# Kernel optimization log

Measured on AMD Instinct MI355X. Metric: run time of the kernel, lower is better.

Reference implementation:

```python
import jax, jax.numpy as jnp
import numpy as np

K = 3        # kernel size
PAD = 1      # padding
DG = 16      # deformable groups
MAXR = 10.0  # max_residue_magnitude


def _lrelu(x):
    return jnp.where(x >= 0, x, 0.1 * x)


def _conv3(x, w, b):
    y = jax.lax.conv_general_dilated(x, w, (1, 1), 'SAME',
                                     dimension_numbers=('NCHW', 'OIHW', 'NCHW'))
    return y + b[None, :, None, None]


def _deform_conv2d(x, offset, mask, weight, bias):
    # x: [B,Cin,H,W]; offset: [B,2*DG*K*K,H,W]; mask: [B,DG*K*K,H,W]
    B, Cin, H, W = x.shape
    Cout = weight.shape[0]
    G, Cg, K2 = DG, Cin // DG, K * K
    off = offset.reshape(B, G, K2, 2, H, W)
    dy, dx = off[:, :, :, 0], off[:, :, :, 1]
    ky = jnp.repeat(jnp.arange(K), K).astype(x.dtype)   # [K2]
    kx = jnp.tile(jnp.arange(K), K).astype(x.dtype)
    hh = jnp.arange(H, dtype=x.dtype)
    ww = jnp.arange(W, dtype=x.dtype)
    # sampling positions [B,G,K2,H,W]
    py = dy + ky[None, None, :, None, None] + hh[None, None, None, :, None] - PAD
    px = dx + kx[None, None, :, None, None] + ww[None, None, None, None, :] - PAD
    y0 = jnp.floor(py)
    x0 = jnp.floor(px)
    wy1 = py - y0
    wx1 = px - x0
    xf = x.reshape(B, G, Cg, H * W)

    def gather(yi, xi, wgt):
        valid = (yi >= 0) & (yi <= H - 1) & (xi >= 0) & (xi <= W - 1)
        idx = (jnp.clip(yi, 0, H - 1).astype(jnp.int32) * W
               + jnp.clip(xi, 0, W - 1).astype(jnp.int32)).reshape(B, G, -1)
        vals = jnp.take_along_axis(
            xf, jnp.broadcast_to(idx[:, :, None, :], (B, G, Cg, idx.shape[-1])), axis=3)
        vals = vals.reshape(B, G, Cg, K2, H, W)
        w = (wgt * valid.astype(x.dtype))[:, :, None]  # [B,G,1,K2,H,W]
        return vals * w

    s = (gather(y0, x0, (1 - wy1) * (1 - wx1))
         + gather(y0, x0 + 1, (1 - wy1) * wx1)
         + gather(y0 + 1, x0, wy1 * (1 - wx1))
         + gather(y0 + 1, x0 + 1, wy1 * wx1))
    s = s * mask.reshape(B, G, K2, H, W)[:, :, None]
    wr = weight.reshape(Cout, G, Cg, K2)
    out = jnp.einsum('ogck,bgckhw->bohw', wr, s)
    return out + bias[None, :, None, None]


def setup_inputs() -> dict:
    key = jax.random.key(0)
    ks = jax.random.split(key, 16)
    B, Cin, Cout, H, W = 4, 128, 64, 96, 96
    Coff = 3 * Cout + 4  # 196
    stdv = 1.0 / np.sqrt(Cin * K * K)
    inp = {
        'x': jax.random.normal(ks[0], (B, Cin, H, W), jnp.float32),
        'extra_feat': jax.random.normal(ks[1], (B, 3 * Cout, H, W), jnp.float32),
        'flow_1': jax.random.normal(ks[2], (B, 2, H, W), jnp.float32),
        'flow_2': jax.random.normal(ks[3], (B, 2, H, W), jnp.float32),
        'weight': jax.random.uniform(ks[4], (Cout, Cin, K, K), jnp.float32, -stdv, stdv),
        'bias': jax.random.normal(ks[5], (Cout,), jnp.float32) * 0.01,
        'ow0': jax.random.normal(ks[6], (Cout, Coff, K, K), jnp.float32) * 0.02,
        'ob0': jnp.zeros((Cout,), jnp.float32),
        'ow1': jax.random.normal(ks[7], (Cout, Cout, K, K), jnp.float32) * 0.02,
        'ob1': jnp.zeros((Cout,), jnp.float32),
        'ow2': jax.random.normal(ks[8], (Cout, Cout, K, K), jnp.float32) * 0.02,
        'ob2': jnp.zeros((Cout,), jnp.float32),
        'ow3': jax.random.normal(ks[9], (27 * DG, Cout, K, K), jnp.float32) * 0.01,
        'ob3': jnp.zeros((27 * DG,), jnp.float32),
    }
    return inp


def reference(x, extra_feat, flow_1, flow_2, weight, bias,
              ow0, ob0, ow1, ob1, ow2, ob2, ow3, ob3):
    feat = jnp.concatenate([extra_feat, flow_1, flow_2], axis=1)
    h = _lrelu(_conv3(feat, ow0, ob0))
    h = _lrelu(_conv3(h, ow1, ob1))
    h = _lrelu(_conv3(h, ow2, ob2))
    out = _conv3(h, ow3, ob3)
    o1, o2, m = jnp.split(out, 3, axis=1)
    offs = MAXR * jnp.tanh(jnp.concatenate([o1, o2], axis=1))
    off1, off2 = jnp.split(offs, 2, axis=1)
    off1 = off1 + jnp.tile(flow_1[:, ::-1], (1, off1.shape[1] // 2, 1, 1))
    off2 = off2 + jnp.tile(flow_2[:, ::-1], (1, off2.shape[1] // 2, 1, 1))
    offset = jnp.concatenate([off1, off2], axis=1)
    mask = jax.nn.sigmoid(m)
    return _deform_conv2d(x, offset, mask, weight, bias)
```

## Files before the change

kernel.cpp:

```cpp
#include <hip/hip_runtime.h>
#include <math.h>

#define HW 9216
#define Hh 96
#define Ww 96
#define PHW 9604

typedef __attribute__((ext_vector_type(8))) short bh8;
typedef __attribute__((ext_vector_type(4))) short bh4;
typedef __attribute__((ext_vector_type(4))) float f32x4;
typedef __attribute__((ext_vector_type(2))) float f32x2;
typedef __attribute__((ext_vector_type(4))) int i32x4;
union bh8i { bh8 v; i32x4 i; };

__device__ __forceinline__ short f2bf(float f) {
    union { float f; unsigned u; } v; v.f = f;
    unsigned r = v.u + 0x7FFFu + ((v.u >> 16) & 1u);
    return (short)(r >> 16);
}
__device__ __forceinline__ float bf2f(short s) {
    union { unsigned u; float f; } v; v.u = ((unsigned)(unsigned short)s) << 16;
    return v.f;
}
__device__ __forceinline__ float lo_bf(unsigned u) {
    union { unsigned u; float f; } v; v.u = u << 16; return v.f;
}
__device__ __forceinline__ float hi_bf(unsigned u) {
    union { unsigned u; float f; } v; v.u = u & 0xFFFF0000u; return v.f;
}
__device__ __forceinline__ int cvt_pk_bf16(float lo, float hi) {
    int r;
    asm("v_cvt_pk_bf16_f32 %0, %1, %2" : "=v"(r) : "v"(lo), "v"(hi));
    return r;
}

__global__ void prep_misc(short* __restrict__ xpad1, short* __restrict__ hpa,
                          short* __restrict__ hpb, short* __restrict__ xdp,
                          const float* __restrict__ ow0, const float* __restrict__ ow1,
                          const float* __restrict__ ow2, const float* __restrict__ ow3,
                          const float* __restrict__ wd,
                          short* __restrict__ wb0, short* __restrict__ wb1,
                          short* __restrict__ wb2, short* __restrict__ wb3,
                          short* __restrict__ wbd) {
    int i = blockIdx.x * 256 + threadIdx.x;
    const int z1 = 4 * 388 * 224, z2 = 4 * 388 * 64;
    if (i < z1 + 2 * z2) {
        short* p; int C;
        if (i < z1) { p = xpad1; C = 224; }
        else if (i < z1 + z2) { p = hpa; C = 64; i -= z1; }
        else { p = hpb; C = 64; i -= z1 + z2; }
        int c = i % C;
        int r = i / C;
        int b = r / 388, pid = r - b * 388;
        int row, col;
        if (pid < 98)       { row = 0;  col = pid; }
        else if (pid < 196) { row = 97; col = pid - 98; }
        else if (pid < 292) { row = pid - 196 + 1; col = 0; }
        else                { row = pid - 292 + 1; col = 97; }
        p[((size_t)b * PHW + row * 98 + col) * C + c] = 0;
        return;
    }
    i -= z1 + 2 * z2;
    const int zr = 4 * 16 * 388 * 8;
    if (i < zr) {
        int c8 = i & 7;
        int r = i >> 3;
        int pid = r % 388;
        int bg = r / 388;
        int row, col;
        if (pid < 98)       { row = 0;  col = pid; }
        else if (pid < 196) { row = 97; col = pid - 98; }
        else if (pid < 292) { row = pid - 196 + 1; col = 0; }
        else                { row = pid - 292 + 1; col = 97; }
        xdp[((size_t)bg * PHW + row * 98 + col) * 8 + c8] = 0;
        return;
    }
    i -= zr;
    const int n0 = 64 * 9 * 224, n1 = 64 * 9 * 64, n3 = 448 * 9 * 64, nd = 64 * 1152;
    if (i < n0) {
        int co = i / (9 * 224); int r = i - co * (9 * 224);
        int tap = r / 224, ci = r - tap * 224;
        wb0[i] = f2bf(ci < 196 ? ow0[(co * 196 + ci) * 9 + tap] : 0.f);
        return;
    }
    i -= n0;
    if (i < n1) {
        int co = i / (9 * 64); int r = i - co * (9 * 64);
        int tap = r / 64, ci = r - tap * 64;
        wb1[i] = f2bf(ow1[(co * 64 + ci) * 9 + tap]);
        return;
    }
    i -= n1;
    if (i < n1) {
        int co = i / (9 * 64); int r = i - co * (9 * 64);
        int tap = r / 64, ci = r - tap * 64;
        wb2[i] = f2bf(ow2[(co * 64 + ci) * 9 + tap]);
        return;
    }
    i -= n1;
    if (i < n3) {
        int co = i / (9 * 64); int r = i - co * (9 * 64);
        int tap = r / 64, ci = r - tap * 64;
        wb3[i] = f2bf(co < 432 ? ow3[(co * 64 + ci) * 9 + tap] : 0.f);
        return;
    }
    i -= n3;
    if (i < nd) {
        int co = i / 1152, kd = i - co * 1152;
        int gt = kd >> 3, c = kd & 7;
        int g = gt / 9, tap = gt - g * 9;
        wbd[i] = f2bf(wd[(co * 128 + g * 8 + c) * 9 + tap]);
    }
}

__global__ void pack_all(const float* __restrict__ extra,
                         const float* __restrict__ f1,
                         const float* __restrict__ f2,
                         const float* __restrict__ x,
                         short* __restrict__ xp,
                         short* __restrict__ xdp) {
    __shared__ float t[32][33];
    const int tid = threadIdx.x, tx = tid & 31, ty = tid >> 5;
    const int pt = blockIdx.x, b = blockIdx.z;
    if (blockIdx.y < 7) {
        const int ct = blockIdx.y;
#pragma unroll
        for (int j = 0; j < 4; ++j) {
            int ch = ct * 32 + ty + j * 8;
            int p = pt * 32 + tx;
            float v = 0.f;
            if (ch < 192)      v = extra[(b * 192 + ch) * HW + p];
            else if (ch < 194) v = f1[(b * 2 + ch - 192) * HW + p];
            else if (ch < 196) v = f2[(b * 2 + ch - 194) * HW + p];
            t[ty + j * 8][tx] = v;
        }
        __syncthreads();
#pragma unroll
        for (int j = 0; j < 4; ++j) {
            int pr = ty + j * 8;
            int p = pt * 32 + pr;
            int r = p / 96, c = p - r * 96;
            xp[((size_t)b * PHW + (r + 1) * 98 + (c + 1)) * 224 + ct * 32 + tx] =
                f2bf(t[tx][pr]);
        }
    } else {
        const int ct = blockIdx.y - 7;
#pragma unroll
        for (int j = 0; j < 4; ++j) {
            int ch = ct * 32 + ty + j * 8;
            t[ty + j * 8][tx] = x[((size_t)b * 128 + ch) * HW + pt * 32 + tx];
        }
        __syncthreads();
        if (tid < 128) {
            int oct = tid >> 5, p = tid & 31;
            int g = ct * 4 + oct;
            int pix = pt * 32 + p;
            int r = pix / 96, c = pix - r * 96;
            bh8 v;
#pragma unroll
            for (int cc = 0; cc < 8; ++cc) v[cc] = f2bf(t[oct * 8 + cc][p]);
            *(bh8*)&xdp[(((size_t)b * 16 + g) * PHW + (r + 1) * 98 + (c + 1)) * 8] = v;
        }
    }
}

template<int CINP, int KCH>
__launch_bounds__(256)
__global__ void conv_mfma(const short* __restrict__ xp,
                          const short* __restrict__ wb,
                          const float* __restrict__ bias,
                          short* __restrict__ o1) {
    __shared__ __attribute__((aligned(16))) short smA[9 * 64 * 32];
    const int tid = threadIdx.x;
    const int lane = tid & 63, wv = tid >> 6;
    const int q = lane >> 4, l15 = lane & 15;
    const int b = blockIdx.y;
    const int pix0 = blockIdx.x * 64 + wv * 16;
    const int soh = pix0 / 96, sow = pix0 - (pix0 / 96) * 96;

    const short* bp = xp + ((size_t)b * PHW + soh * 98 + sow + l15) * CINP + q * 8;

    const int sco = tid >> 2, sqq = tid & 3;
    const short* wsrc = wb + (size_t)sco * (9 * CINP) + sqq * 8;

    f32x4 acc[4];
#pragma unroll
    for (int t = 0; t < 4; ++t) acc[t] = (f32x4){0.f, 0.f, 0.f, 0.f};

    for (int p = 0; p < KCH; ++p) {
        __syncthreads();
        bh8 wtmp[9];
#pragma unroll
        for (int tap = 0; tap < 9; ++tap)
            wtmp[tap] = *(const bh8*)(wsrc + tap * CINP + p * 32);
#pragma unroll
        for (int tap = 0; tap < 9; ++tap)
            *(bh8*)&smA[tap * 2048 + sco * 32 + sqq * 8] = wtmp[tap];
        __syncthreads();
#pragma unroll
        for (int tap = 0; tap < 9; ++tap) {
            const int ky = tap / 3, kx = tap - (tap / 3) * 3;
            bh8 bf = *(const bh8*)(bp + (ky * 98 + kx) * CINP + p * 32);
#pragma unroll
            for (int t = 0; t < 4; ++t) {
                bh8 af = *(const bh8*)&smA[tap * 2048 + (t * 16 + l15) * 32 + q * 8];
                acc[t] = __builtin_amdgcn_mfma_f32_16x16x32_bf16(af, bf, acc[t], 0, 0, 0);
            }
        }
    }

    size_t base = ((size_t)b * PHW + (soh + 1) * 98 + sow + l15 + 1) * 64;
#pragma unroll
    for (int t = 0; t < 4; ++t) {
        bh4 v4;
#pragma unroll
        for (int r = 0; r < 4; ++r) {
            int co = t * 16 + q * 4 + r;
            float v = acc[t][r] + bias[co];
            v = (v >= 0.f) ? v : 0.1f * v;
            v4[r] = f2bf(v);
        }
        *(bh4*)(o1 + base + t * 16 + q * 4) = v4;
    }
}

__launch_bounds__(256)
__global__ void conv4_mfma(const short* __restrict__ xp,
                           const short* __restrict__ wb,
                           const float* __restrict__ bias,
                           float* __restrict__ offp,
                           short* __restrict__ maskb,
                           const float* __restrict__ flow1,
                           const float* __restrict__ flow2) {
    __shared__ __attribute__((aligned(16))) short smA[9 * 64 * 32];
    const int tid = threadIdx.x;
    const int lane = tid & 63, wv = tid >> 6;
    const int q = lane >> 4, l15 = lane & 15;
    const int b = blockIdx.y;
    const int cob = blockIdx.z * 64;
    const int pix0 = blockIdx.x * 64 + wv * 16;
    const int soh = pix0 / 96, sow = pix0 - (pix0 / 96) * 96;

    const short* bp = xp + ((size_t)b * PHW + soh * 98 + sow + l15) * 64 + q * 8;

    const int sco = tid >> 2, sqq = tid & 3;
    const short* wsrc = wb + (size_t)(cob + sco) * 576 + sqq * 8;

    f32x4 acc[4];
#pragma unroll
    for (int t = 0; t < 4; ++t) acc[t] = (f32x4){0.f, 0.f, 0.f, 0.f};

    for (int p = 0; p < 2; ++p) {
        __syncthreads();
        bh8 wtmp[9];
#pragma unroll
        for (int tap = 0; tap < 9; ++tap)
            wtmp[tap] = *(const bh8*)(wsrc + tap * 64 + p * 32);
#pragma unroll
        for (int tap = 0; tap < 9; ++tap)
            *(bh8*)&smA[tap * 2048 + sco * 32 + sqq * 8] = wtmp[tap];
        __syncthreads();
#pragma unroll
        for (int tap = 0; tap < 9; ++tap) {
            const int ky = tap / 3, kx = tap - (tap / 3) * 3;
            bh8 bf = *(const bh8*)(bp + (ky * 98 + kx) * 64 + p * 32);
#pragma unroll
            for (int t = 0; t < 4; ++t) {
                bh8 af = *(const bh8*)&smA[tap * 2048 + (t * 16 + l15) * 32 + q * 8];
                acc[t] = __builtin_amdgcn_mfma_f32_16x16x32_bf16(af, bf, acc[t], 0, 0, 0);
            }
        }
    }

    const int pix = pix0 + l15;
#pragma unroll
    for (int t = 0; t < 4; ++t) {
        int cb0 = cob + t * 16 + q * 4;
        if (cb0 < 288) {
            const float* fl = (cb0 < 144) ? flow1 : flow2;
            float fe = fl[(b * 2 + 1) * HW + pix];
            float fo = fl[(b * 2) * HW + pix];
            float t0 = 10.f * tanhf(acc[t][0] + bias[cb0 + 0]) + fe;
            float t1 = 10.f * tanhf(acc[t][1] + bias[cb0 + 1]) + fo;
            float t2 = 10.f * tanhf(acc[t][2] + bias[cb0 + 2]) + fe;
            float t3 = 10.f * tanhf(acc[t][3] + bias[cb0 + 3]) + fo;
            size_t p0 = ((size_t)b * 144 + (cb0 >> 1)) * HW + pix;
            *(f32x2*)&offp[p0 * 2] = (f32x2){t0, t1};
            *(f32x2*)&offp[(p0 + HW) * 2] = (f32x2){t2, t3};
        } else {
#pragma unroll
            for (int r = 0; r < 4; ++r) {
                int chn = cb0 + r;
                if (chn < 432) {
                    float v = acc[t][r] + bias[chn];
                    maskb[((size_t)b * 144 + (chn - 288)) * HW + pix] =
                        f2bf(1.f / (1.f + expf(-v)));
                }
            }
        }
    }
}

__launch_bounds__(256)
__global__ void deform_mfma(const short* __restrict__ xdp,
                            const float* __restrict__ offp,
                            const short* __restrict__ maskb,
                            const short* __restrict__ wbd,
                            const float* __restrict__ bias,
                            float* __restrict__ out) {
    __shared__ float red[4][1024];
    const int tid = threadIdx.x;
    const int lane = tid & 63, wv = tid >> 6;
    const int q = lane >> 4, l15 = lane & 15;
    const int blk = blockIdx.x;
    const int xs = blk & 7, idx = blk >> 3;
    const int b = xs >> 1;
    const int pix0 = ((xs & 1) * 288 + idx) * 16;
    const int pix = pix0 + l15;
    const int h = pix / 96, w = pix - (pix / 96) * 96;

    const float* opp = offp + ((size_t)b * 144 * HW + pix) * 2;
    const short* mp = maskb + (size_t)b * 144 * HW + pix;
    const short* xb = xdp + (size_t)b * 16 * PHW * 8;
    const short* ap = wbd + (size_t)l15 * 1152 + wv * 288 + q * 8;

    f32x2 dxy[9];
    float mk[9];
#pragma unroll
    for (int i = 0; i < 9; ++i) {
        const int gt = wv * 36 + i * 4 + q;
        dxy[i] = *(const f32x2*)(opp + (size_t)gt * HW * 2);
        mk[i] = bf2f(mp[(size_t)gt * HW]);
    }

    const short* cp[9];
    f32x4 ww[9];
#pragma unroll
    for (int i = 0; i < 9; ++i) {
        const int gt = wv * 36 + i * 4 + q;
        const int g = gt / 9, tap = gt - (gt / 9) * 9;
        float py = dxy[i][0] + (float)(tap / 3) + (float)h - 1.f;
        float px = dxy[i][1] + (float)(tap - (tap / 3) * 3) + (float)w - 1.f;
        py = fminf(fmaxf(py, -1.f), 96.f);
        px = fminf(fmaxf(px, -1.f), 96.f);
        float y0f = floorf(py), x0f = floorf(px);
        float wy1 = py - y0f, wx1 = px - x0f;
        float wy0 = 1.f - wy1, wx0 = 1.f - wx1;
        int yp = (int)y0f + 1, xp = (int)x0f + 1;
        cp[i] = xb + ((size_t)g * PHW + yp * 98 + xp) * 8;
        float m = mk[i];
        ww[i] = (f32x4){wy0 * wx0 * m, wy0 * wx1 * m, wy1 * wx0 * m, wy1 * wx1 * m};
    }

    f32x4 acc[4];
#pragma unroll
    for (int t = 0; t < 4; ++t) acc[t] = (f32x4){0.f, 0.f, 0.f, 0.f};

#pragma unroll
    for (int i = 0; i < 9; ++i) {
        bh8i c00, c01, c10, c11;
        c00.v = *(const bh8*)(cp[i]);
        c01.v = *(const bh8*)(cp[i] + 8);
        c10.v = *(const bh8*)(cp[i] + 98 * 8);
        c11.v = *(const bh8*)(cp[i] + 99 * 8);
        const f32x2 W00 = (f32x2){ww[i][0], ww[i][0]};
        const f32x2 W01 = (f32x2){ww[i][1], ww[i][1]};
        const f32x2 W10 = (f32x2){ww[i][2], ww[i][2]};
        const f32x2 W11 = (f32x2){ww[i][3], ww[i][3]};
        bh8i bf;
#pragma unroll
        for (int k = 0; k < 4; ++k) {
            unsigned u00 = (unsigned)c00.i[k], u01 = (unsigned)c01.i[k];
            unsigned u10 = (unsigned)c10.i[k], u11 = (unsigned)c11.i[k];
            f32x2 p00 = (f32x2){lo_bf(u00), hi_bf(u00)};
            f32x2 p01 = (f32x2){lo_bf(u01), hi_bf(u01)};
            f32x2 p10 = (f32x2){lo_bf(u10), hi_bf(u10)};
            f32x2 p11 = (f32x2){lo_bf(u11), hi_bf(u11)};
            f32x2 s = p00 * W00 + p01 * W01 + p10 * W10 + p11 * W11;
            bf.i[k] = cvt_pk_bf16(s[0], s[1]);
        }
#pragma unroll
        for (int t = 0; t < 4; ++t) {
            bh8 af = *(const bh8*)(ap + (size_t)t * 16 * 1152 + i * 32);
            acc[t] = __builtin_amdgcn_mfma_f32_16x16x32_bf16(af, bf.v, acc[t], 0, 0, 0);
        }
    }

#pragma unroll
    for (int t = 0; t < 4; ++t)
#pragma unroll
        for (int r = 0; r < 4; ++r)
            red[wv][(t * 16 + q * 4 + r) * 16 + l15] = acc[t][r];
    __syncthreads();
    for (int e = tid; e < 1024; e += 256) {
        int co = e >> 4, pl = e & 15;
        float v = red[0][e] + red[1][e] + red[2][e] + red[3][e] + bias[co];
        out[((size_t)b * 64 + co) * HW + pix0 + pl] = v;
    }
}

extern "C" void kernel_launch(void* const* d_in, const int* in_sizes, int n_in,
                              void* d_out, int out_size, void* d_ws, size_t ws_size,
                              hipStream_t stream) {
    const float* x      = (const float*)d_in[0];
    const float* extra  = (const float*)d_in[1];
    const float* flow1  = (const float*)d_in[2];
    const float* flow2  = (const float*)d_in[3];
    const float* weight = (const float*)d_in[4];
    const float* bias   = (const float*)d_in[5];
    const float* ow0    = (const float*)d_in[6];
    const float* ob0    = (const float*)d_in[7];
    const float* ow1    = (const float*)d_in[8];
    const float* ob1    = (const float*)d_in[9];
    const float* ow2    = (const float*)d_in[10];
    const float* ob2    = (const float*)d_in[11];
    const float* ow3    = (const float*)d_in[12];
    const float* ob3    = (const float*)d_in[13];
    float* out = (float*)d_out;

    char* wsb = (char*)d_ws;
    short* xpad1 = (short*)wsb;   wsb += (size_t)4 * PHW * 224 * 2;
    short* hpa   = (short*)wsb;   wsb += (size_t)4 * PHW * 64 * 2;
    short* hpb   = (short*)wsb;   wsb += (size_t)4 * PHW * 64 * 2;
    float* offpair = (float*)wsb; wsb += (size_t)4 * 144 * HW * 2 * 4;
    short* maskbuf = (short*)wsb; wsb += (size_t)4 * 144 * HW * 2;
    short* xdp     = (short*)wsb; wsb += (size_t)4 * 16 * PHW * 8 * 2 + 32;
    short* wb0     = (short*)wsb; wsb += 64 * 9 * 224 * 2;
    short* wb1     = (short*)wsb; wsb += 64 * 9 * 64 * 2;
    short* wb2     = (short*)wsb; wsb += 64 * 9 * 64 * 2;
    short* wb3     = (short*)wsb; wsb += 448 * 9 * 64 * 2;
    short* wbd     = (short*)wsb;

    const int prep_total = 546304 + 198656 + 534528;
    prep_misc<<<dim3((prep_total + 255) / 256), 256, 0, stream>>>(
        xpad1, hpa, hpb, xdp, ow0, ow1, ow2, ow3, weight,
        wb0, wb1, wb2, wb3, wbd);
    pack_all<<<dim3(288, 11, 4), 256, 0, stream>>>(extra, flow1, flow2, x, xpad1, xdp);

    conv_mfma<224, 7><<<dim3(144, 4), 256, 0, stream>>>(xpad1, wb0, ob0, hpa);
    conv_mfma<64, 2><<<dim3(144, 4), 256, 0, stream>>>(hpa, wb1, ob1, hpb);
    conv_mfma<64, 2><<<dim3(144, 4), 256, 0, stream>>>(hpb, wb2, ob2, hpa);
    conv4_mfma<<<dim3(144, 4, 7), 256, 0, stream>>>(hpa, wb3, ob3, offpair,
                                                    maskbuf, flow1, flow2);
    deform_mfma<<<dim3(2304), 256, 0, stream>>>(xdp, offpair, maskbuf, wbd, bias, out);
}
```

Before: 299.5 us.

## Restructure deform conv: waves split pixels, LDS-staged weights, K-split with atomics

```diff
diff --git a/kernel.cpp b/kernel.cpp
--- a/kernel.cpp
+++ b/kernel.cpp
@@ -106,10 +106,11 @@
     }
     i -= n3;
     if (i < nd) {
-        int co = i / 1152, kd = i - co * 1152;
-        int gt = kd >> 3, c = kd & 7;
+        int slab = i >> 11, r = i & 2047;
+        int co = r >> 5, k = r & 31;
+        int gt = slab * 4 + (k >> 3), c8 = k & 7;
         int g = gt / 9, tap = gt - g * 9;
-        wbd[i] = f2bf(wd[(co * 128 + g * 8 + c) * 9 + tap]);
+        wbd[i] = f2bf(wd[(co * 128 + g * 8 + c8) * 9 + tap]);
     }
 }
 
@@ -301,6 +302,31 @@
     }
 }
 
+#define BLEND_MFMA(C0, C1, C2, C3, WWv, CL)                                    \
+    {                                                                          \
+        const f32x2 W00 = (f32x2){(WWv)[0], (WWv)[0]};                         \
+        const f32x2 W01 = (f32x2){(WWv)[1], (WWv)[1]};                         \
+        const f32x2 W10 = (f32x2){(WWv)[2], (WWv)[2]};                         \
+        const f32x2 W11 = (f32x2){(WWv)[3], (WWv)[3]};                         \
+        bh8i bf;                                                               \
+        _Pragma("unroll")                                                      \
+        for (int k = 0; k < 4; ++k) {                                          \
+            unsigned u00 = (unsigned)(C0).i[k], u01 = (unsigned)(C1).i[k];     \
+            unsigned u10 = (unsigned)(C2).i[k], u11 = (unsigned)(C3).i[k];     \
+            f32x2 p00 = (f32x2){lo_bf(u00), hi_bf(u00)};                       \
+            f32x2 p01 = (f32x2){lo_bf(u01), hi_bf(u01)};                       \
+            f32x2 p10 = (f32x2){lo_bf(u10), hi_bf(u10)};                       \
+            f32x2 p11 = (f32x2){lo_bf(u11), hi_bf(u11)};                       \
+            f32x2 s = p00 * W00 + p01 * W01 + p10 * W10 + p11 * W11;           \
+            bf.i[k] = cvt_pk_bf16(s[0], s[1]);                                 \
+        }                                                                      \
+        _Pragma("unroll")                                                      \
+        for (int t = 0; t < 4; ++t) {                                          \
+            bh8 af = *(const bh8*)&smW[(CL) * 2048 + (t * 16 + l15) * 32 + q * 8]; \
+            acc[t] = __builtin_amdgcn_mfma_f32_16x16x32_bf16(af, bf.v, acc[t], 0, 0, 0); \
+        }                                                                      \
+    }
+
 __launch_bounds__(256)
 __global__ void deform_mfma(const short* __restrict__ xdp,
                             const float* __restrict__ offp,
@@ -308,95 +334,106 @@
                             const short* __restrict__ wbd,
                             const float* __restrict__ bias,
                             float* __restrict__ out) {
-    __shared__ float red[4][1024];
+    __shared__ __attribute__((aligned(16))) short smW[3 * 2048];
     const int tid = threadIdx.x;
     const int lane = tid & 63, wv = tid >> 6;
     const int q = lane >> 4, l15 = lane & 15;
     const int blk = blockIdx.x;
     const int xs = blk & 7, idx = blk >> 3;
-    const int b = xs >> 1;
-    const int pix0 = ((xs & 1) * 288 + idx) * 16;
-    const int pix = pix0 + l15;
-    const int h = pix / 96, w = pix - (pix / 96) * 96;
-
-    const float* opp = offp + ((size_t)b * 144 * HW + pix) * 2;
-    const short* mp = maskb + (size_t)b * 144 * HW + pix;
-    const short* xb = xdp + (size_t)b * 16 * PHW * 8;
-    const short* ap = wbd + (size_t)l15 * 1152 + wv * 288 + q * 8;
-
-    f32x2 dxy[9];
-    float mk[9];
-#pragma unroll
-    for (int i = 0; i < 9; ++i) {
-        const int gt = wv * 36 + i * 4 + q;
-        dxy[i] = *(const f32x2*)(opp + (size_t)gt * HW * 2);
-        mk[i] = bf2f(mp[(size_t)gt * HW]);
-    }
-
-    const short* cp[9];
-    f32x4 ww[9];
-#pragma unroll
-    for (int i = 0; i < 9; ++i) {
-        const int gt = wv * 36 + i * 4 + q;
-        const int g = gt / 9, tap = gt - (gt / 9) * 9;
-        float py = dxy[i][0] + (float)(tap / 3) + (float)h - 1.f;
-        float px = dxy[i][1] + (float)(tap - (tap / 3) * 3) + (float)w - 1.f;
-        py = fminf(fmaxf(py, -1.f), 96.f);
-        px = fminf(fmaxf(px, -1.f), 96.f);
-        float y0f = floorf(py), x0f = floorf(px);
-        float wy1 = py - y0f, wx1 = px - x0f;
-        float wy0 = 1.f - wy1, wx0 = 1.f - wx1;
-        int yp = (int)y0f + 1, xp = (int)x0f + 1;
-        cp[i] = xb + ((size_t)g * PHW + yp * 98 + xp) * 8;
-        float m = mk[i];
-        ww[i] = (f32x4){wy0 * wx0 * m, wy0 * wx1 * m, wy1 * wx0 * m, wy1 * wx1 * m};
-    }
+    const int b = xs >> 1, gh = xs & 1;
+    const int pixw = idx * 64 + wv * 16 + l15;
+    const int h = pixw / 96, w = pixw - (pixw / 96) * 96;
+
+    const float* opp = offp + ((size_t)(b * 144 + gh * 72) * HW + pixw) * 2;
+    const short* mp  = maskb + (size_t)(b * 144 + gh * 72) * HW + pixw;
+    const short* xb  = xdp + (size_t)b * 16 * PHW * 8;
+    const short* wsrc = wbd + (size_t)(gh * 18) * 2048 + tid * 8;
 
     f32x4 acc[4];
 #pragma unroll
     for (int t = 0; t < 4; ++t) acc[t] = (f32x4){0.f, 0.f, 0.f, 0.f};
 
-#pragma unroll
-    for (int i = 0; i < 9; ++i) {
-        bh8i c00, c01, c10, c11;
-        c00.v = *(const bh8*)(cp[i]);
-        c01.v = *(const bh8*)(cp[i] + 8);
-        c10.v = *(const bh8*)(cp[i] + 98 * 8);
-        c11.v = *(const bh8*)(cp[i] + 99 * 8);
-        const f32x2 W00 = (f32x2){ww[i][0], ww[i][0]};
-        const f32x2 W01 = (f32x2){ww[i][1], ww[i][1]};
-        const f32x2 W10 = (f32x2){ww[i][2], ww[i][2]};
-        const f32x2 W11 = (f32x2){ww[i][3], ww[i][3]};
-        bh8i bf;
-#pragma unroll
-        for (int k = 0; k < 4; ++k) {
-            unsigned u00 = (unsigned)c00.i[k], u01 = (unsigned)c01.i[k];
-            unsigned u10 = (unsigned)c10.i[k], u11 = (unsigned)c11.i[k];
-            f32x2 p00 = (f32x2){lo_bf(u00), hi_bf(u00)};
-            f32x2 p01 = (f32x2){lo_bf(u01), hi_bf(u01)};
-            f32x2 p10 = (f32x2){lo_bf(u10), hi_bf(u10)};
-            f32x2 p11 = (f32x2){lo_bf(u11), hi_bf(u11)};
-            f32x2 s = p00 * W00 + p01 * W01 + p10 * W10 + p11 * W11;
-            bf.i[k] = cvt_pk_bf16(s[0], s[1]);
-        }
-#pragma unroll
-        for (int t = 0; t < 4; ++t) {
-            bh8 af = *(const bh8*)(ap + (size_t)t * 16 * 1152 + i * 32);
-            acc[t] = __builtin_amdgcn_mfma_f32_16x16x32_bf16(af, bf.v, acc[t], 0, 0, 0);
+    f32x2 dc[3]; float mc[3];
+#pragma unroll
+    for (int cl = 0; cl < 3; ++cl) {
+        int lt = cl * 4 + q;
+        dc[cl] = *(const f32x2*)(opp + (size_t)lt * HW * 2);
+        mc[cl] = bf2f(mp[(size_t)lt * HW]);
+    }
+
+    for (int r = 0; r < 6; ++r) {
+        __syncthreads();
+        bh8 st0 = *(const bh8*)(wsrc + (r * 3 + 0) * 2048);
+        bh8 st1 = *(const bh8*)(wsrc + (r * 3 + 1) * 2048);
+        bh8 st2 = *(const bh8*)(wsrc + (r * 3 + 2) * 2048);
+        *(bh8*)&smW[0 * 2048 + tid * 8] = st0;
+        *(bh8*)&smW[1 * 2048 + tid * 8] = st1;
+        *(bh8*)&smW[2 * 2048 + tid * 8] = st2;
+        __syncthreads();
+
+        f32x2 dn[3]; float mn[3];
+        if (r < 5) {
+#pragma unroll
+            for (int cl = 0; cl < 3; ++cl) {
+                int lt = ((r + 1) * 3 + cl) * 4 + q;
+                dn[cl] = *(const f32x2*)(opp + (size_t)lt * HW * 2);
+                mn[cl] = bf2f(mp[(size_t)lt * HW]);
+            }
+        }
+
+        int soff[3]; f32x4 ww[3];
+#pragma unroll
+        for (int cl = 0; cl < 3; ++cl) {
+            int gt = gh * 72 + (r * 3 + cl) * 4 + q;
+            int g = gt / 9, tap = gt - g * 9;
+            float py = dc[cl][0] + (float)(tap / 3) + (float)h - 1.f;
+            float px = dc[cl][1] + (float)(tap - (tap / 3) * 3) + (float)w - 1.f;
+            py = fminf(fmaxf(py, -1.f), 96.f);
+            px = fminf(fmaxf(px, -1.f), 96.f);
+            float y0f = floorf(py), x0f = floorf(px);
+            float wy1 = py - y0f, wx1 = px - x0f;
+            float wy0 = 1.f - wy1, wx0 = 1.f - wx1;
+            int yp = (int)y0f + 1, xq = (int)x0f + 1;
+            soff[cl] = (g * PHW + yp * 98 + xq) * 8;
+            float m = mc[cl];
+            ww[cl] = (f32x4){wy0 * wx0 * m, wy0 * wx1 * m, wy1 * wx0 * m, wy1 * wx1 * m};
+        }
+
+        bh8i a0, a1, a2, a3, b0, b1, b2, b3;
+        {
+            const short* p = xb + soff[0];
+            a0.v = *(const bh8*)(p);          a1.v = *(const bh8*)(p + 8);
+            a2.v = *(const bh8*)(p + 98 * 8); a3.v = *(const bh8*)(p + 99 * 8);
+        }
+        {
+            const short* p = xb + soff[1];
+            b0.v = *(const bh8*)(p);          b1.v = *(const bh8*)(p + 8);
+            b2.v = *(const bh8*)(p + 98 * 8); b3.v = *(const bh8*)(p + 99 * 8);
+        }
+        BLEND_MFMA(a0, a1, a2, a3, ww[0], 0);
+        {
+            const short* p = xb + soff[2];
+            a0.v = *(const bh8*)(p);          a1.v = *(const bh8*)(p + 8);
+            a2.v = *(const bh8*)(p + 98 * 8); a3.v = *(const bh8*)(p + 99 * 8);
+        }
+        BLEND_MFMA(b0, b1, b2, b3, ww[1], 1);
+        BLEND_MFMA(a0, a1, a2, a3, ww[2], 2);
+
+        if (r < 5) {
+#pragma unroll
+            for (int cl = 0; cl < 3; ++cl) { dc[cl] = dn[cl]; mc[cl] = mn[cl]; }
         }
     }
 
 #pragma unroll
     for (int t = 0; t < 4; ++t)
 #pragma unroll
-        for (int r = 0; r < 4; ++r)
-            red[wv][(t * 16 + q * 4 + r) * 16 + l15] = acc[t][r];
-    __syncthreads();
-    for (int e = tid; e < 1024; e += 256) {
-        int co = e >> 4, pl = e & 15;
-        float v = red[0][e] + red[1][e] + red[2][e] + red[3][e] + bias[co];
-        out[((size_t)b * 64 + co) * HW + pix0 + pl] = v;
-    }
+        for (int rr = 0; rr < 4; ++rr) {
+            int co = t * 16 + q * 4 + rr;
+            float v = acc[t][rr];
+            if (gh == 0) v += bias[co];
+            atomicAdd(&out[((size_t)b * 64 + co) * HW + pixw], v);
+        }
 }
 
 extern "C" void kernel_launch(void* const* d_in, const int* in_sizes, int n_in,
@@ -431,6 +468,8 @@
     short* wb3     = (short*)wsb; wsb += 448 * 9 * 64 * 2;
     short* wbd     = (short*)wsb;
 
+    hipMemsetAsync(out, 0, out_size, stream);
+
     const int prep_total = 546304 + 198656 + 534528;
     prep_misc<<<dim3((prep_total + 255) / 256), 256, 0, stream>>>(
         xpad1, hpa, hpb, xdp, ow0, ow1, ow2, ow3, weight,
@@ -442,5 +481,5 @@
     conv_mfma<64, 2><<<dim3(144, 4), 256, 0, stream>>>(hpb, wb2, ob2, hpa);
     conv4_mfma<<<dim3(144, 4, 7), 256, 0, stream>>>(hpa, wb3, ob3, offpair,
                                                     maskbuf, flow1, flow2);
-    deform_mfma<<<dim3(2304), 256, 0, stream>>>(xdp, offpair, maskbuf, wbd, bias, out);
-}
+    deform_mfma<<<dim3(1152), 256, 0, stream>>>(xdp, offpair, maskbuf, wbd, bias, out);
+}
```

Result: faster. 282.4 us (-5.7%).
